# Performance work log

Hardware: AMD Instinct MI355X
Metric: run time of the kernel (lower is better)

The kernel has to match this reference:

```python
import jax, jax.numpy as jnp
import numpy as np
import math

N, L, D = 1024, 32, 768
N_OUT, IN_DIM, OUT_DIM = 16, 64, 64
EPS = 1e-8


def setup_inputs() -> dict:
    key = jax.random.key(0)
    ks = jax.random.split(key, 4)
    x = jax.random.normal(ks[0], (N, L, D), jnp.float32)
    mask = jnp.ones((N, L), jnp.float32)
    scaled = lambda k, shape, fan: jax.random.normal(k, shape, jnp.float32) * (1.0 / np.sqrt(fan).astype(np.float32))
    Wscore = scaled(ks[1], (L, D, 1), D)
    Bscore = jnp.zeros((L, 1, 1), jnp.float32)
    Wcap = scaled(ks[2], (L, D, IN_DIM), D)
    Bcap = jnp.zeros((L, 1, IN_DIM), jnp.float32)
    Wvote = scaled(ks[3], (L, N_OUT, IN_DIM, OUT_DIM), IN_DIM)
    Bvote = jnp.zeros((L, N_OUT, 1, OUT_DIM), jnp.float32)
    beta_use = jnp.zeros((L, 1, 1, 1), jnp.float32)
    beta_ign = jnp.zeros((1, N_OUT, 1, 1), jnp.float32)
    return dict(x=x, mask=mask, Wscore=Wscore, Bscore=Bscore, Wcap=Wcap,
                Bcap=Bcap, Wvote=Wvote, Bvote=Bvote, beta_use=beta_use,
                beta_ign=beta_ign, iters=3)


def reference(x, mask, Wscore, Bscore, Wcap, Bcap, Wvote, Bvote, beta_use, beta_ign, iters):
    n_out = Wvote.shape[1]
    half_pi = np.float32(0.5 * math.pi)
    x_t = jnp.transpose(x, (1, 0, 2))                      # [L, N, D]
    a_in = jnp.matmul(x_t, Wscore) + Bscore                # [L, N, 1]
    mu_in = jax.nn.gelu(jnp.matmul(x_t, Wcap) + Bcap, approximate=False)  # [L, N, in_dim]
    f_a_in = jax.nn.sigmoid(a_in) * jnp.transpose(mask)[..., None]        # [L, N, 1]
    f_a_in = f_a_in[:, None, :, :]                         # [L, 1, N, 1]
    # votes: [L, n_out, N, out_dim] (einsum avoids materializing repeated mu_in)
    V = jnp.einsum('lni,lkio->lkno', mu_in, Wvote) + Bvote

    R = jnp.full((1, n_out, 1, 1), 1.0 / n_out, dtype=x.dtype)
    a_out = mu_out = var_out = None
    for t in range(iters):
        if t > 0:
            log_p = (-jnp.sum((V - mu_out[None]) ** 2 / (2.0 * var_out[None] + EPS), axis=-1)
                     - 1.0 - half_pi
                     - 0.5 * jnp.sum(jnp.log(var_out[None] + EPS), axis=-1))   # [L, n_out, N]
            R = jax.nn.softmax(jax.nn.log_sigmoid(a_out)[None] + log_p[..., None], axis=1)
        D_use = f_a_in * R                                  # [L, n_out, N, 1]
        D_ign = f_a_in - D_use
        a_out = jnp.sum(beta_use * D_use, axis=0) - jnp.sum(beta_ign * D_ign, axis=0)  # [n_out, N, 1]
        denom = jnp.sum(D_use, axis=0) + EPS                # [n_out, N, 1]
        mu_out = jnp.sum(D_use * V, axis=0) / denom         # [n_out, N, out_dim]
        var_out = jnp.sum(D_use * (V - mu_out[None]) ** 2, axis=0) / denom

    a_fin = jnp.transpose(a_out[..., 0])                    # [N, n_out]
    mu_fin = jnp.transpose(mu_out, (1, 0, 2))               # [N, n_out, out_dim]
    return a_fin, mu_fin
```

## Files before the change

### kernel.cpp

```cpp
#include <hip/hip_runtime.h>
#include <hip/hip_bf16.h>

#define L_DIM 32
#define N_DIM 1024
#define D_DIM 768
#define K_DIM 16
#define I_DIM 64
#define O_DIM 64
#define EPSF 1e-8f
#define PX 72

typedef unsigned short u16;
typedef __attribute__((ext_vector_type(8))) short short8;
typedef __attribute__((ext_vector_type(4))) float f32x4;
#define MFMA __builtin_amdgcn_mfma_f32_16x16x32_bf16

__device__ __forceinline__ float bf2f(u16 v) {
    union { unsigned int u; float f; } x; x.u = ((unsigned int)v) << 16; return x.f;
}
__device__ __forceinline__ u16 f2bf(float f) {
    union { float f; unsigned int u; } x; x.f = f;
    unsigned int u = x.u;
    u += 0x7FFFu + ((u >> 16) & 1u);
    return (u16)(u >> 16);
}
__device__ __forceinline__ void split2(float v, u16& h, u16& l) {
    u16 hh = f2bf(v);
    h = hh;
    l = f2bf(v - bf2f(hh));
}
__device__ __forceinline__ void store_split4(u16* ph, u16* pl, float4 v) {
    unsigned u0 = __float_as_uint(v.x), u1 = __float_as_uint(v.y);
    unsigned u2 = __float_as_uint(v.z), u3 = __float_as_uint(v.w);
    uint2 H, L;
    H.x = (u0 >> 16) | (u1 & 0xFFFF0000u);
    H.y = (u2 >> 16) | (u3 & 0xFFFF0000u);
    float l0 = v.x - __uint_as_float(u0 & 0xFFFF0000u);
    float l1 = v.y - __uint_as_float(u1 & 0xFFFF0000u);
    float l2 = v.z - __uint_as_float(u2 & 0xFFFF0000u);
    float l3 = v.w - __uint_as_float(u3 & 0xFFFF0000u);
    L.x = (__float_as_uint(l0) >> 16) | (__float_as_uint(l1) & 0xFFFF0000u);
    L.y = (__float_as_uint(l2) >> 16) | (__float_as_uint(l3) & 0xFFFF0000u);
    *(uint2*)ph = H;
    *(uint2*)pl = L;
}

__global__ __launch_bounds__(256) void prep_w(
    const float* __restrict__ Wc, u16* __restrict__ cH, u16* __restrict__ cL,
    const float* __restrict__ Wv, u16* __restrict__ vH, u16* __restrict__ vL)
{
    const int l = blockIdx.y, t = threadIdx.x;
    __shared__ float tile[64][65];
    if (blockIdx.x < 12) {
        const int d0 = blockIdx.x * 64;
        #pragma unroll
        for (int p = 0; p < 4; p++) {
            int dd = p * 16 + (t >> 4), i4 = (t & 15) * 4;
            float4 v = *(const float4*)&Wc[((size_t)l * D_DIM + d0 + dd) * I_DIM + i4];
            tile[dd][i4] = v.x; tile[dd][i4+1] = v.y; tile[dd][i4+2] = v.z; tile[dd][i4+3] = v.w;
        }
        __syncthreads();
        #pragma unroll
        for (int p = 0; p < 4; p++) {
            int i = p * 16 + (t >> 4), dd0 = (t & 15) * 4;
            u16 h[4], lo[4];
            #pragma unroll
            for (int j = 0; j < 4; j++) split2(tile[dd0 + j][i], h[j], lo[j]);
            size_t base = ((size_t)l * I_DIM + i) * D_DIM + d0 + dd0;
            uint2 ph; ph.x = h[0] | ((unsigned)h[1] << 16); ph.y = h[2] | ((unsigned)h[3] << 16);
            uint2 pl; pl.x = lo[0] | ((unsigned)lo[1] << 16); pl.y = lo[2] | ((unsigned)lo[3] << 16);
            *(uint2*)&cH[base] = ph;
            *(uint2*)&cL[base] = pl;
        }
    } else {
        const int k = blockIdx.x - 12;
        #pragma unroll
        for (int p = 0; p < 4; p++) {
            int i = p * 16 + (t >> 4), o4 = (t & 15) * 4;
            float4 v = *(const float4*)&Wv[(((size_t)l * K_DIM + k) * I_DIM + i) * O_DIM + o4];
            tile[i][o4] = v.x; tile[i][o4+1] = v.y; tile[i][o4+2] = v.z; tile[i][o4+3] = v.w;
        }
        __syncthreads();
        #pragma unroll
        for (int p = 0; p < 4; p++) {
            int o = p * 16 + (t >> 4), i0 = (t & 15) * 4;
            u16 h[4], lo[4];
            #pragma unroll
            for (int j = 0; j < 4; j++) split2(tile[i0 + j][o], h[j], lo[j]);
            size_t base = (((size_t)l * K_DIM + k) * O_DIM + o) * I_DIM + i0;
            uint2 ph; ph.x = h[0] | ((unsigned)h[1] << 16); ph.y = h[2] | ((unsigned)h[3] << 16);
            uint2 pl; pl.x = lo[0] | ((unsigned)lo[1] << 16); pl.y = lo[2] | ((unsigned)lo[3] << 16);
            *(uint2*)&vH[base] = ph;
            *(uint2*)&vL[base] = pl;
        }
    }
}

#define A_CHUNK(K0, R0, R1, WH0, WL0, WH1, WL1, BUF)                        \
  {                                                                          \
    const float* wp = &wsc_s[(K0) + sd];                                     \
    fa0 += R0.x * wp[0] + R0.y * wp[1] + R0.z * wp[2] + R0.w * wp[3];        \
    fa1 += R1.x * wp[0] + R1.y * wp[1] + R1.z * wp[2] + R1.w * wp[3];        \
    store_split4(&xh[BUF][sg][sd],      &xl[BUF][sg][sd],      R0);          \
    store_split4(&xh[BUF][16 + sg][sd], &xl[BUF][16 + sg][sd], R1);          \
    __syncthreads();                                                         \
    if ((K0) + 128 < D_DIM) {                                                \
      R0 = *(const float4*)&x[xoff0 + (K0) + 128 + sd];                      \
      R1 = *(const float4*)&x[xoff1 + (K0) + 128 + sd];                      \
    }                                                                        \
    {                                                                        \
      short8 bh, bl;                                                         \
      bh = *(const short8*)&xh[BUF][ln16][quad * 8];                         \
      bl = *(const short8*)&xl[BUF][ln16][quad * 8];                         \
      acc0 = MFMA(WH0, bh, acc0, 0, 0, 0);                                   \
      acc0 = MFMA(WH0, bl, acc0, 0, 0, 0);                                   \
      acc0 = MFMA(WL0, bh, acc0, 0, 0, 0);                                   \
      bh = *(const short8*)&xh[BUF][16 + ln16][quad * 8];                    \
      bl = *(const short8*)&xl[BUF][16 + ln16][quad * 8];                    \
      acc1 = MFMA(WH0, bh, acc1, 0, 0, 0);                                   \
      acc1 = MFMA(WH0, bl, acc1, 0, 0, 0);                                   \
      acc1 = MFMA(WL0, bh, acc1, 0, 0, 0);                                   \
      bh = *(const short8*)&xh[BUF][ln16][32 + quad * 8];                    \
      bl = *(const short8*)&xl[BUF][ln16][32 + quad * 8];                    \
      acc0 = MFMA(WH1, bh, acc0, 0, 0, 0);                                   \
      acc0 = MFMA(WH1, bl, acc0, 0, 0, 0);                                   \
      acc0 = MFMA(WL1, bh, acc0, 0, 0, 0);                                   \
      bh = *(const short8*)&xh[BUF][16 + ln16][32 + quad * 8];               \
      bl = *(const short8*)&xl[BUF][16 + ln16][32 + quad * 8];               \
      acc1 = MFMA(WH1, bh, acc1, 0, 0, 0);                                   \
      acc1 = MFMA(WH1, bl, acc1, 0, 0, 0);                                   \
      acc1 = MFMA(WL1, bh, acc1, 0, 0, 0);                                   \
    }                                                                        \
    if ((K0) + 128 < D_DIM) {                                                \
      WH0 = *(const short8*)&WcH[wrow + (K0) + 128];                         \
      WL0 = *(const short8*)&WcL[wrow + (K0) + 128];                         \
      WH1 = *(const short8*)&WcH[wrow + (K0) + 160];                         \
      WL1 = *(const short8*)&WcL[wrow + (K0) + 160];                         \
    }                                                                        \
  }

__global__ __launch_bounds__(256, 4) void kernelA(
    const float* __restrict__ x, const float* __restrict__ mask,
    const float* __restrict__ Wscore, const float* __restrict__ Bscore,
    const u16* __restrict__ WcH, const u16* __restrict__ WcL,
    const float* __restrict__ Bcap,
    float* __restrict__ mu_out, float* __restrict__ fa_out,
    int nbase, int nchunk)
{
    const int bid  = blockIdx.y * gridDim.x + blockIdx.x;
    const int slot = bid >> 3;
    const int l    = (bid & 7) + 8 * (slot & 3);
    const int n0l  = (slot >> 2) * 32;

    const int t    = threadIdx.x;
    const int w    = t >> 6;
    const int lane = t & 63;
    const int quad = lane >> 4;
    const int ln16 = lane & 15;

    __shared__ u16 xh[2][32][PX], xl[2][32][PX];
    __shared__ float wsc_s[D_DIM];
    __shared__ float bcap_s[64];

    for (int i = t; i < D_DIM; i += 256) wsc_s[i] = Wscore[l * D_DIM + i];
    if (t < 64) bcap_s[t] = Bcap[l * I_DIM + t];

    const int sg = t >> 4;
    const int sd = (t & 15) * 4;

    const size_t xoff0 = ((size_t)(nbase + n0l + sg) * L_DIM + l) * D_DIM;
    const size_t xoff1 = ((size_t)(nbase + n0l + 16 + sg) * L_DIM + l) * D_DIM;

    float4 r0a = *(const float4*)&x[xoff0 + sd];
    float4 r1a = *(const float4*)&x[xoff1 + sd];
    float4 r0b = *(const float4*)&x[xoff0 + 64 + sd];
    float4 r1b = *(const float4*)&x[xoff1 + 64 + sd];

    const size_t wrow = ((size_t)l * I_DIM + (w * 16 + ln16)) * D_DIM + quad * 8;
    short8 wha0 = *(const short8*)&WcH[wrow];
    short8 wla0 = *(const short8*)&WcL[wrow];
    short8 wha1 = *(const short8*)&WcH[wrow + 32];
    short8 wla1 = *(const short8*)&WcL[wrow + 32];
    short8 whb0 = *(const short8*)&WcH[wrow + 64];
    short8 wlb0 = *(const short8*)&WcL[wrow + 64];
    short8 whb1 = *(const short8*)&WcH[wrow + 96];
    short8 wlb1 = *(const short8*)&WcL[wrow + 96];

    __syncthreads();

    f32x4 acc0 = {0.f, 0.f, 0.f, 0.f};
    f32x4 acc1 = {0.f, 0.f, 0.f, 0.f};
    float fa0 = 0.f, fa1 = 0.f;

    #pragma unroll
    for (int cc = 0; cc < 6; cc++) {
        A_CHUNK(cc * 128,      r0a, r1a, wha0, wla0, wha1, wla1, 0)
        A_CHUNK(cc * 128 + 64, r0b, r1b, whb0, wlb0, whb1, wlb1, 1)
    }

    fa0 += __shfl_xor(fa0, 1, 64); fa1 += __shfl_xor(fa1, 1, 64);
    fa0 += __shfl_xor(fa0, 2, 64); fa1 += __shfl_xor(fa1, 2, 64);
    fa0 += __shfl_xor(fa0, 4, 64); fa1 += __shfl_xor(fa1, 4, 64);
    fa0 += __shfl_xor(fa0, 8, 64); fa1 += __shfl_xor(fa1, 8, 64);
    if ((t & 15) == 0) {
        float bs = Bscore[l];
        {
            float a = fa0 + bs;
            float sig = 1.f / (1.f + expf(-a));
            float m = mask[(size_t)(nbase + n0l + sg) * L_DIM + l];
            fa_out[(size_t)l * nchunk + n0l + sg] = sig * m;
        }
        {
            float a = fa1 + bs;
            float sig = 1.f / (1.f + expf(-a));
            float m = mask[(size_t)(nbase + n0l + 16 + sg) * L_DIM + l];
            fa_out[(size_t)l * nchunk + n0l + 16 + sg] = sig * m;
        }
    }

    #pragma unroll
    for (int c = 0; c < 2; c++) {
        const f32x4 a = (c == 0) ? acc0 : acc1;
        const int n = c * 16 + ln16;
        const int i0 = w * 16 + quad * 4;
        float4 o;
        float* op = (float*)&o;
        #pragma unroll
        for (int r = 0; r < 4; r++) {
            float v = a[r] + bcap_s[i0 + r];
            op[r] = 0.5f * v * (1.f + erff(v * 0.70710678118f));
        }
        *(float4*)&mu_out[((size_t)l * nchunk + n0l + n) * I_DIM + i0] = o;
    }
}

__global__ __launch_bounds__(256) void kernelB(
    const float* __restrict__ mu_in,
    const u16* __restrict__ WvH, const u16* __restrict__ WvL,
    const float* __restrict__ Bvote,
    float* __restrict__ V, int nchunk)
{
    const int bid  = (blockIdx.z * gridDim.y + blockIdx.y) * gridDim.x + blockIdx.x;
    const int slot = bid >> 3;
    const int l    = (bid & 7) + 8 * (slot & 3);
    const int rem  = slot >> 2;
    const int k    = rem & 15;
    const int n0l  = (rem >> 4) * 64;

    const int t    = threadIdx.x;
    const int w    = t >> 6;
    const int lane = t & 63;
    const int quad = lane >> 4;
    const int ln16 = lane & 15;

    __shared__ u16 mh[64][PX], ml[64][PX];
    __shared__ float bvote_s[64];

    const int srow = t >> 4, scol = (t & 15) * 4;
    float4 m0 = *(const float4*)&mu_in[((size_t)l * nchunk + n0l + srow) * I_DIM + scol];
    float4 m1 = *(const float4*)&mu_in[((size_t)l * nchunk + n0l + 16 + srow) * I_DIM + scol];
    float4 m2 = *(const float4*)&mu_in[((size_t)l * nchunk + n0l + 32 + srow) * I_DIM + scol];
    float4 m3 = *(const float4*)&mu_in[((size_t)l * nchunk + n0l + 48 + srow) * I_DIM + scol];

    const size_t wrow = (((size_t)l * K_DIM + k) * O_DIM + (w * 16 + ln16)) * I_DIM + quad * 8;
    short8 ah0 = *(const short8*)&WvH[wrow];
    short8 al0 = *(const short8*)&WvL[wrow];
    short8 ah1 = *(const short8*)&WvH[wrow + 32];
    short8 al1 = *(const short8*)&WvL[wrow + 32];

    if (t < 64) bvote_s[t] = Bvote[((size_t)l * K_DIM + k) * O_DIM + t];

    store_split4(&mh[srow][scol],      &ml[srow][scol],      m0);
    store_split4(&mh[16 + srow][scol], &ml[16 + srow][scol], m1);
    store_split4(&mh[32 + srow][scol], &ml[32 + srow][scol], m2);
    store_split4(&mh[48 + srow][scol], &ml[48 + srow][scol], m3);
    __syncthreads();

    f32x4 acc[4] = {{0.f,0.f,0.f,0.f},{0.f,0.f,0.f,0.f},{0.f,0.f,0.f,0.f},{0.f,0.f,0.f,0.f}};

    #pragma unroll
    for (int c = 0; c < 4; c++) {
        const int n = c * 16 + ln16;
        short8 bh = *(const short8*)&mh[n][quad * 8];
        short8 bl = *(const short8*)&ml[n][quad * 8];
        acc[c] = MFMA(ah0, bh, acc[c], 0, 0, 0);
        acc[c] = MFMA(ah0, bl, acc[c], 0, 0, 0);
        acc[c] = MFMA(al0, bh, acc[c], 0, 0, 0);
    }
    #pragma unroll
    for (int c = 0; c < 4; c++) {
        const int n = c * 16 + ln16;
        short8 bh = *(const short8*)&mh[n][32 + quad * 8];
        short8 bl = *(const short8*)&ml[n][32 + quad * 8];
        acc[c] = MFMA(ah1, bh, acc[c], 0, 0, 0);
        acc[c] = MFMA(ah1, bl, acc[c], 0, 0, 0);
        acc[c] = MFMA(al1, bh, acc[c], 0, 0, 0);
    }

    #pragma unroll
    for (int c = 0; c < 4; c++) {
        const int n = c * 16 + ln16;
        const int o0 = w * 16 + quad * 4;
        float4 o;
        o.x = acc[c][0] + bvote_s[o0];
        o.y = acc[c][1] + bvote_s[o0 + 1];
        o.z = acc[c][2] + bvote_s[o0 + 2];
        o.w = acc[c][3] + bvote_s[o0 + 3];
        *(float4*)&V[(((size_t)(n0l + n) * L_DIM + l) * K_DIM + k) * O_DIM + o0] = o;
    }
}

__global__ __launch_bounds__(512, 4) void kernelC(
    const float* __restrict__ V, const float* __restrict__ fa_in,
    const float* __restrict__ beta_use, const float* __restrict__ beta_ign,
    const int* __restrict__ iters_p,
    float* __restrict__ out, int nbase, int nchunk)
{
    const int nl   = blockIdx.x;
    const int ng   = nbase + nl;
    const int t    = threadIdx.x;
    const int k    = t >> 5;
    const int op   = t & 31;
    const int o0   = op * 2;
    const int lane = t & 63;
    int iters = iters_p[0];
    if (iters < 0 || iters > 16) iters = 3;

    __shared__ float sc_s[32][17];
    __shared__ float Rfa_s[16][36];
    __shared__ float RfaBu_s[16][36];

    const float* Vb = &V[(size_t)nl * (L_DIM * K_DIM * O_DIM)];
    float2 Vr[32];
    #pragma unroll
    for (int l = 0; l < 32; l++)
        Vr[l] = *(const float2*)&Vb[(l * K_DIM + k) * O_DIM + o0];

    const int lrow = t >> 4;
    const int kcol = t & 15;
    const float fa_l = fa_in[(size_t)lrow * nchunk + nl];
    const float bu_l = beta_use[lrow];
    const float bi_k = beta_ign[k];

    Rfa_s[kcol][lrow]   = fa_l * (1.f / 16.f);
    RfaBu_s[kcol][lrow] = fa_l * bu_l * (1.f / 16.f);
    __syncthreads();

    float mu0 = 0.f, mu1 = 0.f, var0 = 0.f, var1 = 0.f, a_r = 0.f;
    float Sfa = 0.f;

    for (int it = 0; it < iters; it++) {
        if (it > 0) {
            float g0 = 1.f / (2.f * var0 + EPSF);
            float g1 = 1.f / (2.f * var1 + EPSF);
            float lvp = logf(var0 + EPSF) + logf(var1 + EPSF);
            lvp += __shfl_xor(lvp, 1, 64);
            lvp += __shfl_xor(lvp, 2, 64);
            lvp += __shfl_xor(lvp, 4, 64);
            lvp += __shfl_xor(lvp, 8, 64);
            lvp += __shfl_xor(lvp, 16, 64);
            float ls = fminf(a_r, 0.f) - log1pf(expf(-fabsf(a_r)));
            const float cst = ls - 1.f - 1.57079632679f - 0.5f * lvp;

            const bool s16 = (lane & 16) != 0;
            const bool s8  = (lane & 8)  != 0;
            const bool s4  = (lane & 4)  != 0;
            const bool s2  = (lane & 2)  != 0;
            const bool s1  = (lane & 1)  != 0;
            float w16[16];
            #pragma unroll
            for (int j = 0; j < 16; j++) {
                float d0 = Vr[j].x - mu0,      d1 = Vr[j].y - mu1;
                float a  = d0 * d0 * g0 + d1 * d1 * g1;
                float e0 = Vr[j + 16].x - mu0, e1 = Vr[j + 16].y - mu1;
                float b  = e0 * e0 * g0 + e1 * e1 * g1;
                float ta = a + __shfl_xor(a, 16, 64);
                float tb = b + __shfl_xor(b, 16, 64);
                w16[j] = s16 ? tb : ta;
            }
            float w8[8];
            #pragma unroll
            for (int j = 0; j < 8; j++) {
                float ta = w16[j]     + __shfl_xor(w16[j],     8, 64);
                float tb = w16[j + 8] + __shfl_xor(w16[j + 8], 8, 64);
                w8[j] = s8 ? tb : ta;
            }
            float w4[4];
            #pragma unroll
            for (int j = 0; j < 4; j++) {
                float ta = w8[j]     + __shfl_xor(w8[j],     4, 64);
                float tb = w8[j + 4] + __shfl_xor(w8[j + 4], 4, 64);
                w4[j] = s4 ? tb : ta;
            }
            float w2[2];
            #pragma unroll
            for (int j = 0; j < 2; j++) {
                float ta = w4[j]     + __shfl_xor(w4[j],     2, 64);
                float tb = w4[j + 2] + __shfl_xor(w4[j + 2], 2, 64);
                w2[j] = s2 ? tb : ta;
            }
            float ta = w2[0] + __shfl_xor(w2[0], 1, 64);
            float tb = w2[1] + __shfl_xor(w2[1], 1, 64);
            float w1 = s1 ? tb : ta;
            sc_s[lane & 31][k] = cst - w1;
            __syncthreads();

            {
                float s0 = sc_s[lrow][kcol];
                float m = s0;
                m = fmaxf(m, __shfl_xor(m, 1, 64));
                m = fmaxf(m, __shfl_xor(m, 2, 64));
                m = fmaxf(m, __shfl_xor(m, 4, 64));
                m = fmaxf(m, __shfl_xor(m, 8, 64));
                float e = expf(s0 - m);
                float sum = e;
                sum += __shfl_xor(sum, 1, 64);
                sum += __shfl_xor(sum, 2, 64);
                sum += __shfl_xor(sum, 4, 64);
                sum += __shfl_xor(sum, 8, 64);
                float R = e / sum;
                float rf = R * fa_l;
                Rfa_s[kcol][lrow]   = rf;
                RfaBu_s[kcol][lrow] = rf * bu_l;
            }
            __syncthreads();
        }
        float denom = EPSF, sbu = 0.f;
        float mua0 = 0.f, mua1 = 0.f, v2a0 = 0.f, v2a1 = 0.f;
        #pragma unroll
        for (int l4 = 0; l4 < 8; l4++) {
            const float4 rf = *(const float4*)&Rfa_s[k][l4 * 4];
            const float4 rb = *(const float4*)&RfaBu_s[k][l4 * 4];
            const float* rfp = (const float*)&rf;
            const float* rbp = (const float*)&rb;
            #pragma unroll
            for (int j = 0; j < 4; j++) {
                const int l = l4 * 4 + j;
                float Du = rfp[j];
                denom += Du;
                sbu   += rbp[j];
                float dv0 = Du * Vr[l].x;
                float dv1 = Du * Vr[l].y;
                mua0 += dv0;  v2a0 += dv0 * Vr[l].x;
                mua1 += dv1;  v2a1 += dv1 * Vr[l].y;
            }
        }
        if (it == 0) Sfa = (denom - EPSF) * 16.f;
        a_r = sbu + bi_k * ((denom - EPSF) - Sfa);
        float invd = 1.f / denom;
        mu0 = mua0 * invd;
        mu1 = mua1 * invd;
        var0 = fmaxf(v2a0 * invd - mu0 * mu0, 0.f);
        var1 = fmaxf(v2a1 * invd - mu1 * mu1, 0.f);
    }

    if (op == 0) out[(size_t)ng * K_DIM + k] = a_r;
    float2 o2; o2.x = mu0; o2.y = mu1;
    *(float2*)&out[(size_t)N_DIM * K_DIM + ((size_t)ng * K_DIM + k) * O_DIM + o0] = o2;
}

extern "C" void kernel_launch(void* const* d_in, const int* in_sizes, int n_in,
                              void* d_out, int out_size, void* d_ws, size_t ws_size,
                              hipStream_t stream) {
    (void)out_size;
    static const int EXP[11] = {25165824, 32768, 24576, 32, 1572864, 64,
                                2097152, 65536, 32, 16, 1};
    int mapi[11];
    bool used[64] = {false};
    for (int s = 0; s < 11; s++) {
        mapi[s] = (s < n_in) ? s : 0;
        for (int j = 0; j < n_in && j < 64; j++) {
            if (!used[j] && in_sizes[j] == EXP[s]) { mapi[s] = j; used[j] = true; break; }
        }
    }
    const float* x        = (const float*)d_in[mapi[0]];
    const float* mask     = (const float*)d_in[mapi[1]];
    const float* Wscore   = (const float*)d_in[mapi[2]];
    const float* Bscore   = (const float*)d_in[mapi[3]];
    const float* Wcap     = (const float*)d_in[mapi[4]];
    const float* Bcap     = (const float*)d_in[mapi[5]];
    const float* Wvote    = (const float*)d_in[mapi[6]];
    const float* Bvote    = (const float*)d_in[mapi[7]];
    const float* beta_use = (const float*)d_in[mapi[8]];
    const float* beta_ign = (const float*)d_in[mapi[9]];
    const int*   iters    = (const int*)d_in[mapi[10]];
    float* out = (float*)d_out;

    const size_t WCAP = (size_t)L_DIM * I_DIM * D_DIM;
    const size_t WVOT = (size_t)L_DIM * K_DIM * O_DIM * I_DIM;
    const size_t WBYTES = 2 * WCAP * 2 + 2 * WVOT * 2;

    int C = 64;
    {
        const int cands[5] = {1024, 512, 256, 128, 64};
        for (int i = 0; i < 5; i++) {
            size_t need = WBYTES + (size_t)cands[i] * (128 + 8192 + 131072);
            if (need <= ws_size) { C = cands[i]; break; }
        }
    }

    char* ws = (char*)d_ws;
    u16* WcH = (u16*)ws;
    u16* WcL = (u16*)(ws + WCAP * 2);
    u16* WvH = (u16*)(ws + WCAP * 4);
    u16* WvL = (u16*)(ws + WCAP * 4 + WVOT * 2);
    char* dyn = ws + WBYTES;
    float* fa = (float*)dyn;
    float* mu = (float*)(dyn + (size_t)128 * C);
    float* V  = (float*)(dyn + (size_t)128 * C + (size_t)8192 * C);

    prep_w<<<dim3(28, 32), 256, 0, stream>>>(Wcap, WcH, WcL, Wvote, WvH, WvL);

    for (int nbase = 0; nbase < N_DIM; nbase += C) {
        kernelA<<<dim3(C / 32, 32), 256, 0, stream>>>(
            x, mask, Wscore, Bscore, WcH, WcL, Bcap, mu, fa, nbase, C);
        kernelB<<<dim3(C / 64, 16, 32), 256, 0, stream>>>(
            mu, WvH, WvL, Bvote, V, C);
        kernelC<<<dim3(C), 512, 0, stream>>>(
            V, fa, beta_use, beta_ign, iters, out, nbase, C);
    }
}
```

Before: 304.5 us.

## Process four output capsules per kernelB block and relayout V as [L,K,N,O]

kernelB now handles four k values per block, so the mu_in tile is loaded and split into bf16 hi/lo only once per four k and reused. Weight loads for the next k are double-buffered in registers to overlap with the MFMAs. V is stored as [L][K][N][O] instead of [N][L][K][O], which makes kernelB writes contiguous along n, and kernelC's reads are changed to match. In exchange kernelC's per-block V reads become strided across L and K, the grid is four times smaller, and register pressure rises.

After: 303.3 us. About the same (-0.4%).

```diff
diff --git a/kernel.cpp b/kernel.cpp
--- a/kernel.cpp
+++ b/kernel.cpp
@@ -234,6 +234,49 @@
     }
 }
 
+#define B_STEP(KK, AH0, AL0, AH1, AL1, NH0, NL0, NH1, NL1, PRE)              \
+  {                                                                          \
+    if (PRE) {                                                               \
+      const size_t wn = wrow0 + (size_t)((KK) + 1) * (O_DIM * I_DIM);        \
+      NH0 = *(const short8*)&WvH[wn];                                        \
+      NL0 = *(const short8*)&WvL[wn];                                        \
+      NH1 = *(const short8*)&WvH[wn + 32];                                   \
+      NL1 = *(const short8*)&WvL[wn + 32];                                   \
+    }                                                                        \
+    f32x4 acc[4] = {{0.f,0.f,0.f,0.f},{0.f,0.f,0.f,0.f},                     \
+                    {0.f,0.f,0.f,0.f},{0.f,0.f,0.f,0.f}};                    \
+    _Pragma("unroll")                                                        \
+    for (int c = 0; c < 4; c++) {                                            \
+        const int n = c * 16 + ln16;                                         \
+        short8 bh = *(const short8*)&mh[n][quad * 8];                        \
+        short8 bl = *(const short8*)&ml[n][quad * 8];                        \
+        acc[c] = MFMA(AH0, bh, acc[c], 0, 0, 0);                             \
+        acc[c] = MFMA(AH0, bl, acc[c], 0, 0, 0);                             \
+        acc[c] = MFMA(AL0, bh, acc[c], 0, 0, 0);                             \
+    }                                                                        \
+    _Pragma("unroll")                                                        \
+    for (int c = 0; c < 4; c++) {                                            \
+        const int n = c * 16 + ln16;                                         \
+        short8 bh = *(const short8*)&mh[n][32 + quad * 8];                   \
+        short8 bl = *(const short8*)&ml[n][32 + quad * 8];                   \
+        acc[c] = MFMA(AH1, bh, acc[c], 0, 0, 0);                             \
+        acc[c] = MFMA(AH1, bl, acc[c], 0, 0, 0);                             \
+        acc[c] = MFMA(AL1, bh, acc[c], 0, 0, 0);                             \
+    }                                                                        \
+    _Pragma("unroll")                                                        \
+    for (int c = 0; c < 4; c++) {                                            \
+        const int n = c * 16 + ln16;                                         \
+        const int o0 = w * 16 + quad * 4;                                    \
+        float4 o;                                                            \
+        o.x = acc[c][0] + bvote_s[KK][o0];                                   \
+        o.y = acc[c][1] + bvote_s[KK][o0 + 1];                               \
+        o.z = acc[c][2] + bvote_s[KK][o0 + 2];                               \
+        o.w = acc[c][3] + bvote_s[KK][o0 + 3];                               \
+        *(float4*)&V[(((size_t)l * K_DIM + k0 + (KK)) * nchunk + n0l + n)    \
+                     * O_DIM + o0] = o;                                      \
+    }                                                                        \
+  }
+
 __global__ __launch_bounds__(256) void kernelB(
     const float* __restrict__ mu_in,
     const u16* __restrict__ WvH, const u16* __restrict__ WvL,
@@ -244,8 +287,9 @@
     const int slot = bid >> 3;
     const int l    = (bid & 7) + 8 * (slot & 3);
     const int rem  = slot >> 2;
-    const int k    = rem & 15;
-    const int n0l  = (rem >> 4) * 64;
+    const int kg   = rem & 3;
+    const int n0l  = (rem >> 2) * 64;
+    const int k0   = kg * 4;
 
     const int t    = threadIdx.x;
     const int w    = t >> 6;
@@ -254,7 +298,7 @@
     const int ln16 = lane & 15;
 
     __shared__ u16 mh[64][PX], ml[64][PX];
-    __shared__ float bvote_s[64];
+    __shared__ float bvote_s[4][64];
 
     const int srow = t >> 4, scol = (t & 15) * 4;
     float4 m0 = *(const float4*)&mu_in[((size_t)l * nchunk + n0l + srow) * I_DIM + scol];
@@ -262,13 +306,14 @@
     float4 m2 = *(const float4*)&mu_in[((size_t)l * nchunk + n0l + 32 + srow) * I_DIM + scol];
     float4 m3 = *(const float4*)&mu_in[((size_t)l * nchunk + n0l + 48 + srow) * I_DIM + scol];
 
-    const size_t wrow = (((size_t)l * K_DIM + k) * O_DIM + (w * 16 + ln16)) * I_DIM + quad * 8;
-    short8 ah0 = *(const short8*)&WvH[wrow];
-    short8 al0 = *(const short8*)&WvL[wrow];
-    short8 ah1 = *(const short8*)&WvH[wrow + 32];
-    short8 al1 = *(const short8*)&WvL[wrow + 32];
-
-    if (t < 64) bvote_s[t] = Bvote[((size_t)l * K_DIM + k) * O_DIM + t];
+    const size_t wrow0 = (((size_t)l * K_DIM + k0) * O_DIM + (w * 16 + ln16)) * I_DIM + quad * 8;
+    short8 ha0 = *(const short8*)&WvH[wrow0];
+    short8 la0 = *(const short8*)&WvL[wrow0];
+    short8 ha1 = *(const short8*)&WvH[wrow0 + 32];
+    short8 la1 = *(const short8*)&WvL[wrow0 + 32];
+    short8 hb0, lb0, hb1, lb1;
+
+    bvote_s[t >> 6][t & 63] = Bvote[((size_t)l * K_DIM + k0 + (t >> 6)) * O_DIM + (t & 63)];
 
     store_split4(&mh[srow][scol],      &ml[srow][scol],      m0);
     store_split4(&mh[16 + srow][scol], &ml[16 + srow][scol], m1);
@@ -276,38 +321,10 @@
     store_split4(&mh[48 + srow][scol], &ml[48 + srow][scol], m3);
     __syncthreads();
 
-    f32x4 acc[4] = {{0.f,0.f,0.f,0.f},{0.f,0.f,0.f,0.f},{0.f,0.f,0.f,0.f},{0.f,0.f,0.f,0.f}};
-
-    #pragma unroll
-    for (int c = 0; c < 4; c++) {
-        const int n = c * 16 + ln16;
-        short8 bh = *(const short8*)&mh[n][quad * 8];
-        short8 bl = *(const short8*)&ml[n][quad * 8];
-        acc[c] = MFMA(ah0, bh, acc[c], 0, 0, 0);
-        acc[c] = MFMA(ah0, bl, acc[c], 0, 0, 0);
-        acc[c] = MFMA(al0, bh, acc[c], 0, 0, 0);
-    }
-    #pragma unroll
-    for (int c = 0; c < 4; c++) {
-        const int n = c * 16 + ln16;
-        short8 bh = *(const short8*)&mh[n][32 + quad * 8];
-        short8 bl = *(const short8*)&ml[n][32 + quad * 8];
-        acc[c] = MFMA(ah1, bh, acc[c], 0, 0, 0);
-        acc[c] = MFMA(ah1, bl, acc[c], 0, 0, 0);
-        acc[c] = MFMA(al1, bh, acc[c], 0, 0, 0);
-    }
-
-    #pragma unroll
-    for (int c = 0; c < 4; c++) {
-        const int n = c * 16 + ln16;
-        const int o0 = w * 16 + quad * 4;
-        float4 o;
-        o.x = acc[c][0] + bvote_s[o0];
-        o.y = acc[c][1] + bvote_s[o0 + 1];
-        o.z = acc[c][2] + bvote_s[o0 + 2];
-        o.w = acc[c][3] + bvote_s[o0 + 3];
-        *(float4*)&V[(((size_t)(n0l + n) * L_DIM + l) * K_DIM + k) * O_DIM + o0] = o;
-    }
+    B_STEP(0, ha0, la0, ha1, la1, hb0, lb0, hb1, lb1, 1)
+    B_STEP(1, hb0, lb0, hb1, lb1, ha0, la0, ha1, la1, 1)
+    B_STEP(2, ha0, la0, ha1, la1, hb0, lb0, hb1, lb1, 1)
+    B_STEP(3, hb0, lb0, hb1, lb1, ha0, la0, ha1, la1, 0)
 }
 
 __global__ __launch_bounds__(512, 4) void kernelC(
@@ -330,11 +347,10 @@
     __shared__ float Rfa_s[16][36];
     __shared__ float RfaBu_s[16][36];
 
-    const float* Vb = &V[(size_t)nl * (L_DIM * K_DIM * O_DIM)];
     float2 Vr[32];
     #pragma unroll
     for (int l = 0; l < 32; l++)
-        Vr[l] = *(const float2*)&Vb[(l * K_DIM + k) * O_DIM + o0];
+        Vr[l] = *(const float2*)&V[(((size_t)l * K_DIM + k) * nchunk + nl) * O_DIM + o0];
 
     const int lrow = t >> 4;
     const int kcol = t & 15;
@@ -514,7 +530,7 @@
     for (int nbase = 0; nbase < N_DIM; nbase += C) {
         kernelA<<<dim3(C / 32, 32), 256, 0, stream>>>(
             x, mask, Wscore, Bscore, WcH, WcL, Bcap, mu, fa, nbase, C);
-        kernelB<<<dim3(C / 64, 16, 32), 256, 0, stream>>>(
+        kernelB<<<dim3(C / 64, 4, 32), 256, 0, stream>>>(
             mu, WvH, WvL, Bvote, V, C);
         kernelC<<<dim3(C), 512, 0, stream>>>(
             V, fa, beta_use, beta_ign, iters, out, nbase, C);
```

## Restructure kernelA to stage full 16-row x tile and relayout V by l,k

Applied to the files above, without the earlier changes.

kernelA now handles 16 rows per block instead of 32. It loads the whole 768-wide x row slab into registers up front, splits it into bf16 hi/lo in a 12-chunk shared buffer, and then runs the MFMA loop reading Wcap directly from global with no per-chunk syncs. The launch-bounds occupancy hint drops to 2 and the grid doubles. Separately, the V layout changes to [l][k][n][o], so kernelB writes contiguous rows across n, while kernelC's per-n reads become strided across l,k. This trades a software-pipelined double-buffered loop for higher memory-level parallelism, at the cost of more registers and shared memory and less reuse of W per block.

Result: slower. 334.1 us (+9.7%).

```diff
diff --git a/kernel.cpp b/kernel.cpp
--- a/kernel.cpp
+++ b/kernel.cpp
@@ -96,50 +96,7 @@
     }
 }
 
-#define A_CHUNK(K0, R0, R1, WH0, WL0, WH1, WL1, BUF)                        \
-  {                                                                          \
-    const float* wp = &wsc_s[(K0) + sd];                                     \
-    fa0 += R0.x * wp[0] + R0.y * wp[1] + R0.z * wp[2] + R0.w * wp[3];        \
-    fa1 += R1.x * wp[0] + R1.y * wp[1] + R1.z * wp[2] + R1.w * wp[3];        \
-    store_split4(&xh[BUF][sg][sd],      &xl[BUF][sg][sd],      R0);          \
-    store_split4(&xh[BUF][16 + sg][sd], &xl[BUF][16 + sg][sd], R1);          \
-    __syncthreads();                                                         \
-    if ((K0) + 128 < D_DIM) {                                                \
-      R0 = *(const float4*)&x[xoff0 + (K0) + 128 + sd];                      \
-      R1 = *(const float4*)&x[xoff1 + (K0) + 128 + sd];                      \
-    }                                                                        \
-    {                                                                        \
-      short8 bh, bl;                                                         \
-      bh = *(const short8*)&xh[BUF][ln16][quad * 8];                         \
-      bl = *(const short8*)&xl[BUF][ln16][quad * 8];                         \
-      acc0 = MFMA(WH0, bh, acc0, 0, 0, 0);                                   \
-      acc0 = MFMA(WH0, bl, acc0, 0, 0, 0);                                   \
-      acc0 = MFMA(WL0, bh, acc0, 0, 0, 0);                                   \
-      bh = *(const short8*)&xh[BUF][16 + ln16][quad * 8];                    \
-      bl = *(const short8*)&xl[BUF][16 + ln16][quad * 8];                    \
-      acc1 = MFMA(WH0, bh, acc1, 0, 0, 0);                                   \
-      acc1 = MFMA(WH0, bl, acc1, 0, 0, 0);                                   \
-      acc1 = MFMA(WL0, bh, acc1, 0, 0, 0);                                   \
-      bh = *(const short8*)&xh[BUF][ln16][32 + quad * 8];                    \
-      bl = *(const short8*)&xl[BUF][ln16][32 + quad * 8];                    \
-      acc0 = MFMA(WH1, bh, acc0, 0, 0, 0);                                   \
-      acc0 = MFMA(WH1, bl, acc0, 0, 0, 0);                                   \
-      acc0 = MFMA(WL1, bh, acc0, 0, 0, 0);                                   \
-      bh = *(const short8*)&xh[BUF][16 + ln16][32 + quad * 8];               \
-      bl = *(const short8*)&xl[BUF][16 + ln16][32 + quad * 8];               \
-      acc1 = MFMA(WH1, bh, acc1, 0, 0, 0);                                   \
-      acc1 = MFMA(WH1, bl, acc1, 0, 0, 0);                                   \
-      acc1 = MFMA(WL1, bh, acc1, 0, 0, 0);                                   \
-    }                                                                        \
-    if ((K0) + 128 < D_DIM) {                                                \
-      WH0 = *(const short8*)&WcH[wrow + (K0) + 128];                         \
-      WL0 = *(const short8*)&WcL[wrow + (K0) + 128];                         \
-      WH1 = *(const short8*)&WcH[wrow + (K0) + 160];                         \
-      WL1 = *(const short8*)&WcL[wrow + (K0) + 160];                         \
-    }                                                                        \
-  }
-
-__global__ __launch_bounds__(256, 4) void kernelA(
+__global__ __launch_bounds__(256, 2) void kernelA(
     const float* __restrict__ x, const float* __restrict__ mask,
     const float* __restrict__ Wscore, const float* __restrict__ Bscore,
     const u16* __restrict__ WcH, const u16* __restrict__ WcL,
@@ -150,7 +107,7 @@
     const int bid  = blockIdx.y * gridDim.x + blockIdx.x;
     const int slot = bid >> 3;
     const int l    = (bid & 7) + 8 * (slot & 3);
-    const int n0l  = (slot >> 2) * 32;
+    const int n0l  = (slot >> 2) * 16;
 
     const int t    = threadIdx.x;
     const int w    = t >> 6;
@@ -158,7 +115,7 @@
     const int quad = lane >> 4;
     const int ln16 = lane & 15;
 
-    __shared__ u16 xh[2][32][PX], xl[2][32][PX];
+    __shared__ u16 xh[12][16][PX], xl[12][16][PX];
     __shared__ float wsc_s[D_DIM];
     __shared__ float bcap_s[64];
 
@@ -168,70 +125,62 @@
     const int sg = t >> 4;
     const int sd = (t & 15) * 4;
 
-    const size_t xoff0 = ((size_t)(nbase + n0l + sg) * L_DIM + l) * D_DIM;
-    const size_t xoff1 = ((size_t)(nbase + n0l + 16 + sg) * L_DIM + l) * D_DIM;
-
-    float4 r0a = *(const float4*)&x[xoff0 + sd];
-    float4 r1a = *(const float4*)&x[xoff1 + sd];
-    float4 r0b = *(const float4*)&x[xoff0 + 64 + sd];
-    float4 r1b = *(const float4*)&x[xoff1 + 64 + sd];
+    const size_t xoff = ((size_t)(nbase + n0l + sg) * L_DIM + l) * D_DIM;
+
+    float4 xr[12];
+    #pragma unroll
+    for (int ch = 0; ch < 12; ch++)
+        xr[ch] = *(const float4*)&x[xoff + ch * 64 + sd];
+
+    __syncthreads();
+
+    float fa = 0.f;
+    #pragma unroll
+    for (int ch = 0; ch < 12; ch++) {
+        const float* wp = &wsc_s[ch * 64 + sd];
+        fa += xr[ch].x * wp[0] + xr[ch].y * wp[1] + xr[ch].z * wp[2] + xr[ch].w * wp[3];
+        store_split4(&xh[ch][sg][sd], &xl[ch][sg][sd], xr[ch]);
+    }
+
+    fa += __shfl_xor(fa, 1, 64);
+    fa += __shfl_xor(fa, 2, 64);
+    fa += __shfl_xor(fa, 4, 64);
+    fa += __shfl_xor(fa, 8, 64);
+    if ((t & 15) == 0) {
+        float a = fa + Bscore[l];
+        float sig = 1.f / (1.f + expf(-a));
+        float m = mask[(size_t)(nbase + n0l + sg) * L_DIM + l];
+        fa_out[(size_t)l * nchunk + n0l + sg] = sig * m;
+    }
+
+    __syncthreads();
 
     const size_t wrow = ((size_t)l * I_DIM + (w * 16 + ln16)) * D_DIM + quad * 8;
-    short8 wha0 = *(const short8*)&WcH[wrow];
-    short8 wla0 = *(const short8*)&WcL[wrow];
-    short8 wha1 = *(const short8*)&WcH[wrow + 32];
-    short8 wla1 = *(const short8*)&WcL[wrow + 32];
-    short8 whb0 = *(const short8*)&WcH[wrow + 64];
-    short8 wlb0 = *(const short8*)&WcL[wrow + 64];
-    short8 whb1 = *(const short8*)&WcH[wrow + 96];
-    short8 wlb1 = *(const short8*)&WcL[wrow + 96];
-
-    __syncthreads();
-
-    f32x4 acc0 = {0.f, 0.f, 0.f, 0.f};
-    f32x4 acc1 = {0.f, 0.f, 0.f, 0.f};
-    float fa0 = 0.f, fa1 = 0.f;
-
-    #pragma unroll
-    for (int cc = 0; cc < 6; cc++) {
-        A_CHUNK(cc * 128,      r0a, r1a, wha0, wla0, wha1, wla1, 0)
-        A_CHUNK(cc * 128 + 64, r0b, r1b, whb0, wlb0, whb1, wlb1, 1)
-    }
-
-    fa0 += __shfl_xor(fa0, 1, 64); fa1 += __shfl_xor(fa1, 1, 64);
-    fa0 += __shfl_xor(fa0, 2, 64); fa1 += __shfl_xor(fa1, 2, 64);
-    fa0 += __shfl_xor(fa0, 4, 64); fa1 += __shfl_xor(fa1, 4, 64);
-    fa0 += __shfl_xor(fa0, 8, 64); fa1 += __shfl_xor(fa1, 8, 64);
-    if ((t & 15) == 0) {
-        float bs = Bscore[l];
-        {
-            float a = fa0 + bs;
-            float sig = 1.f / (1.f + expf(-a));
-            float m = mask[(size_t)(nbase + n0l + sg) * L_DIM + l];
-            fa_out[(size_t)l * nchunk + n0l + sg] = sig * m;
-        }
-        {
-            float a = fa1 + bs;
-            float sig = 1.f / (1.f + expf(-a));
-            float m = mask[(size_t)(nbase + n0l + 16 + sg) * L_DIM + l];
-            fa_out[(size_t)l * nchunk + n0l + 16 + sg] = sig * m;
-        }
-    }
-
-    #pragma unroll
-    for (int c = 0; c < 2; c++) {
-        const f32x4 a = (c == 0) ? acc0 : acc1;
-        const int n = c * 16 + ln16;
-        const int i0 = w * 16 + quad * 4;
-        float4 o;
-        float* op = (float*)&o;
-        #pragma unroll
-        for (int r = 0; r < 4; r++) {
-            float v = a[r] + bcap_s[i0 + r];
-            op[r] = 0.5f * v * (1.f + erff(v * 0.70710678118f));
-        }
-        *(float4*)&mu_out[((size_t)l * nchunk + n0l + n) * I_DIM + i0] = o;
-    }
+    f32x4 acc = {0.f, 0.f, 0.f, 0.f};
+    #pragma unroll
+    for (int ch = 0; ch < 12; ch++) {
+        #pragma unroll
+        for (int ks = 0; ks < 2; ks++) {
+            const int kk = ks * 32;
+            short8 ah = *(const short8*)&WcH[wrow + ch * 64 + kk];
+            short8 al = *(const short8*)&WcL[wrow + ch * 64 + kk];
+            short8 bh = *(const short8*)&xh[ch][ln16][kk + quad * 8];
+            short8 bl = *(const short8*)&xl[ch][ln16][kk + quad * 8];
+            acc = MFMA(ah, bh, acc, 0, 0, 0);
+            acc = MFMA(ah, bl, acc, 0, 0, 0);
+            acc = MFMA(al, bh, acc, 0, 0, 0);
+        }
+    }
+
+    const int i0 = w * 16 + quad * 4;
+    float4 o;
+    float* op = (float*)&o;
+    #pragma unroll
+    for (int r = 0; r < 4; r++) {
+        float v = acc[r] + bcap_s[i0 + r];
+        op[r] = 0.5f * v * (1.f + erff(v * 0.70710678118f));
+    }
+    *(float4*)&mu_out[((size_t)l * nchunk + n0l + ln16) * I_DIM + i0] = o;
 }
 
 __global__ __launch_bounds__(256) void kernelB(
@@ -306,7 +255,7 @@
         o.y = acc[c][1] + bvote_s[o0 + 1];
         o.z = acc[c][2] + bvote_s[o0 + 2];
         o.w = acc[c][3] + bvote_s[o0 + 3];
-        *(float4*)&V[(((size_t)(n0l + n) * L_DIM + l) * K_DIM + k) * O_DIM + o0] = o;
+        *(float4*)&V[(((size_t)l * K_DIM + k) * nchunk + n0l + n) * O_DIM + o0] = o;
     }
 }
 
@@ -330,11 +279,10 @@
     __shared__ float Rfa_s[16][36];
     __shared__ float RfaBu_s[16][36];
 
-    const float* Vb = &V[(size_t)nl * (L_DIM * K_DIM * O_DIM)];
     float2 Vr[32];
     #pragma unroll
     for (int l = 0; l < 32; l++)
-        Vr[l] = *(const float2*)&Vb[(l * K_DIM + k) * O_DIM + o0];
+        Vr[l] = *(const float2*)&V[(((size_t)l * K_DIM + k) * nchunk + nl) * O_DIM + o0];
 
     const int lrow = t >> 4;
     const int kcol = t & 15;
@@ -512,7 +460,7 @@
     prep_w<<<dim3(28, 32), 256, 0, stream>>>(Wcap, WcH, WcL, Wvote, WvH, WvL);
 
     for (int nbase = 0; nbase < N_DIM; nbase += C) {
-        kernelA<<<dim3(C / 32, 32), 256, 0, stream>>>(
+        kernelA<<<dim3(C / 16, 32), 256, 0, stream>>>(
             x, mask, Wscore, Bscore, WcH, WcL, Bcap, mu, fa, nbase, C);
         kernelB<<<dim3(C / 64, 16, 32), 256, 0, stream>>>(
             mu, WvH, WvL, Bvote, V, C);
```
